# Optimization experiments

Hardware: AMD Instinct MI355X
Metric: run time of the kernel (lower is better)

## Reference

```python
import jax, jax.numpy as jnp
import numpy as np

N = 100000   # nodes
E = 1600000  # edges
IN_DIM, HID, HEADS, OUT_DIM = 8, 64, 4, 3


def _add_self_loops(src, dst, n):
    loop = jnp.arange(n, dtype=src.dtype)
    return jnp.concatenate([src, loop]), jnp.concatenate([dst, loop])


def gcn_conv(x, src, dst, n, W, b):
    # PyG GCNConv: add self-loops, symmetric normalization deg^-1/2 * deg^-1/2
    s, d = _add_self_loops(src, dst, n)
    deg = jax.ops.segment_sum(jnp.ones(s.shape[0], x.dtype), d, num_segments=n)
    dinv = jnp.where(deg > 0, jax.lax.rsqrt(deg), 0.0)
    norm = dinv[s] * dinv[d]                       # [E']
    h = x @ W                                      # [N, out]
    out = jax.ops.segment_sum(norm[:, None] * h[s], d, num_segments=n)
    return out + b


def gat_conv(x, src, dst, n, W, att_src, att_dst, b):
    # PyG GATConv, concat=True, negative_slope=0.2, self-loops added
    h = (x @ W).reshape(n, HEADS, HID)             # [N, H, C]
    s, d = _add_self_loops(src, dst, n)
    a_src = jnp.sum(h * att_src, axis=-1)          # [N, H]
    a_dst = jnp.sum(h * att_dst, axis=-1)          # [N, H]
    e = jax.nn.leaky_relu(a_src[s] + a_dst[d], negative_slope=0.2)  # [E', H]
    m = jax.lax.stop_gradient(jax.ops.segment_max(e, d, num_segments=n))
    ex = jnp.exp(e - m[d])
    denom = jax.ops.segment_sum(ex, d, num_segments=n)
    alpha = ex / (denom[d] + 1e-16)                # segment softmax over incoming edges
    out = jax.ops.segment_sum(alpha[:, :, None] * h[s], d, num_segments=n)  # [N, H, C]
    return out.reshape(n, HEADS * HID) + b


def setup_inputs() -> dict:
    key = jax.random.key(0)
    ks = jax.random.split(key, 16)
    def glorot(k, shape):
        fan = shape[0] + shape[-1]
        return jax.random.normal(k, shape, jnp.float32) * np.sqrt(2.0 / fan)
    return {
        "x": jax.random.normal(ks[0], (N, IN_DIM), jnp.float32),
        "edge_index": jax.random.randint(ks[1], (2, E), 0, N, jnp.int64 if jax.config.jax_enable_x64 else jnp.int32),
        "w1": glorot(ks[2], (IN_DIM, HID)), "b1": jnp.zeros((HID,), jnp.float32),
        "w2": glorot(ks[3], (HID, HID)),   "b2": jnp.zeros((HID,), jnp.float32),
        "w3": glorot(ks[4], (HID, HID)),   "b3": jnp.zeros((HID,), jnp.float32),
        "wg": glorot(ks[5], (HID, HEADS * HID)), "bg": jnp.zeros((HEADS * HID,), jnp.float32),
        "att_src": glorot(ks[6], (HEADS, HID)),
        "att_dst": glorot(ks[7], (HEADS, HID)),
        "wc1": glorot(ks[8], (HEADS * HID, HID)), "bc1": jnp.zeros((HID,), jnp.float32),
        "wc2": glorot(ks[9], (HID, OUT_DIM)),     "bc2": jnp.zeros((OUT_DIM,), jnp.float32),
    }


def reference(x, edge_index, w1, b1, w2, b2, w3, b3, wg, bg, att_src, att_dst, wc1, bc1, wc2, bc2):
    src, dst = edge_index[0], edge_index[1]
    n = x.shape[0]
    # stacked GCN convs with ReLU; residual when shapes match (layers 2,3)
    h = jax.nn.relu(gcn_conv(x, src, dst, n, w1, b1))
    h = h + jax.nn.relu(gcn_conv(h, src, dst, n, w2, b2))
    h = h + jax.nn.relu(gcn_conv(h, src, dst, n, w3, b3))
    # GAT attention layer (4 heads, concat)
    h_att = gat_conv(h, src, dst, n, wg, att_src, att_dst, bg)  # [N, 256]
    # classifier MLP (dropout is inference no-op)
    z = jax.nn.relu(h_att @ wc1 + bc1)
    logits = z @ wc2 + bc2
    return jax.nn.log_softmax(logits, axis=1)
```

## Files before the change

### kernel.cpp

```cpp
#include <hip/hip_runtime.h>
#include <math.h>


typedef _Float16 half8 __attribute__((ext_vector_type(8)));
typedef _Float16 f16x8 __attribute__((ext_vector_type(8)));
typedef float f32x4 __attribute__((ext_vector_type(4)));

__device__ __forceinline__ float leaky02(float v) { return v > 0.f ? v : 0.2f * v; }


template <int CTRL>
__device__ __forceinline__ float dpp_add(float v) {
    int iv = __builtin_bit_cast(int, v);
    int r = __builtin_amdgcn_update_dpp(iv, iv, CTRL, 0xF, 0xF, false);
    return v + __builtin_bit_cast(float, r);
}
template <int OFF>
__device__ __forceinline__ float swz_add(float v) {
    int r = __builtin_amdgcn_ds_swizzle(__builtin_bit_cast(int, v), OFF);
    return v + __builtin_bit_cast(float, r);
}
template <int CTRL>
__device__ __forceinline__ float dpp_max(float v) {
    int iv = __builtin_bit_cast(int, v);
    int r = __builtin_amdgcn_update_dpp(iv, iv, CTRL, 0xF, 0xF, false);
    return fmaxf(v, __builtin_bit_cast(float, r));
}
template <int OFF>
__device__ __forceinline__ float swz_max(float v) {
    int r = __builtin_amdgcn_ds_swizzle(__builtin_bit_cast(int, v), OFF);
    return fmaxf(v, __builtin_bit_cast(float, r));
}
__device__ __forceinline__ float red8(float v) {
    v = dpp_add<0xB1>(v);
    v = dpp_add<0x4E>(v);
    v = swz_add<0x101F>(v);
    return v;
}
__device__ __forceinline__ float red16(float v) {
    v = dpp_add<0xB1>(v);
    v = dpp_add<0x4E>(v);
    v = swz_add<0x101F>(v);
    v = dpp_add<0x128>(v);
    return v;
}
__device__ __forceinline__ float red64(float v) {
    v = dpp_add<0xB1>(v);
    v = dpp_add<0x4E>(v);
    v = swz_add<0x101F>(v);
    v = dpp_add<0x128>(v);
    v = swz_add<0x401F>(v);
    v = v + __shfl_xor(v, 32);
    return v;
}
__device__ __forceinline__ float red64max(float v) {
    v = dpp_max<0xB1>(v);
    v = dpp_max<0x4E>(v);
    v = swz_max<0x101F>(v);
    v = dpp_max<0x128>(v);
    v = swz_max<0x401F>(v);
    v = fmaxf(v, __shfl_xor(v, 32));
    return v;
}


__global__ void count_kernel(const int* __restrict__ dst, int E, int range,
                             int* __restrict__ counts) {
    int grp = blockIdx.x & 7;
    int nlo = grp * range;
    int nhi = nlo + range;
    int nblk = gridDim.x >> 3;
    int c = blockIdx.x >> 3;
    int stride = nblk * blockDim.x;
    for (int e = c * blockDim.x + threadIdx.x; e < E; e += stride) {
        int d = dst[e];
        if (d >= nlo && d < nhi) atomicAdd(&counts[d], 1);
    }
}

__global__ void scan_pass1(const int* __restrict__ counts, int n, int* __restrict__ blockSums) {
    __shared__ int sh[256];
    int base = blockIdx.x * 2048;
    int tid = threadIdx.x;
    int s = 0;
#pragma unroll
    for (int j = 0; j < 8; ++j) {
        int idx = base + tid * 8 + j;
        if (idx < n) s += counts[idx];
    }
    sh[tid] = s;
    __syncthreads();
    for (int off = 128; off > 0; off >>= 1) {
        if (tid < off) sh[tid] += sh[tid + off];
        __syncthreads();
    }
    if (tid == 0) blockSums[blockIdx.x] = sh[0];
}

__global__ void scan_pass2(const int* __restrict__ blockSums, int nb, int* __restrict__ blockOffs) {
    if (threadIdx.x == 0 && blockIdx.x == 0) {
        int run = 0;
        for (int i = 0; i < nb; ++i) { blockOffs[i] = run; run += blockSums[i]; }
    }
}

__global__ void scan_pass3(const int* __restrict__ counts, int n,
                           const int* __restrict__ blockOffs,
                           const float* __restrict__ x,
                           int* __restrict__ row_ptr, int* __restrict__ cursor,
                           float* __restrict__ dinv, float* __restrict__ rdinv,
                           _Float16* __restrict__ xs) {
    __shared__ int sh[256];
    int base = blockIdx.x * 2048;
    int tid = threadIdx.x;
    int cnt[8];
    int local = 0;
#pragma unroll
    for (int j = 0; j < 8; ++j) {
        int idx = base + tid * 8 + j;
        cnt[j] = (idx < n) ? counts[idx] : 0;
        local += cnt[j];
    }
    sh[tid] = local;
    __syncthreads();
    for (int off = 1; off < 256; off <<= 1) {
        int v = (tid >= off) ? sh[tid - off] : 0;
        __syncthreads();
        sh[tid] += v;
        __syncthreads();
    }
    int run = blockOffs[blockIdx.x] + sh[tid] - local;
#pragma unroll
    for (int j = 0; j < 8; ++j) {
        int idx = base + tid * 8 + j;
        if (idx < n) {
            row_ptr[idx] = run;
            cursor[idx] = run;
            float dv = rsqrtf((float)(cnt[j] + 1));
            dinv[idx] = dv;
            rdinv[idx] = sqrtf((float)(cnt[j] + 1));
#pragma unroll
            for (int t = 0; t < 8; ++t) xs[idx * 8 + t] = (_Float16)(dv * x[idx * 8 + t]);
            run += cnt[j];
            if (idx == n - 1) row_ptr[n] = run;
        }
    }
}

__global__ void scatter_kernel(const int* __restrict__ src, const int* __restrict__ dst,
                               int E, int range,
                               int* __restrict__ cursor, int* __restrict__ col_src) {
    int grp = blockIdx.x & 7;
    int nlo = grp * range;
    int nhi = nlo + range;
    int nblk = gridDim.x >> 3;
    int c = blockIdx.x >> 3;
    int stride = nblk * blockDim.x;
    for (int e = c * blockDim.x + threadIdx.x; e < E; e += stride) {
        int d = dst[e];
        if (d >= nlo && d < nhi) {
            int pos = atomicAdd(&cursor[d], 1);
            col_src[pos] = src[e];
        }
    }
}


__global__ void ccomb_kernel(const float* __restrict__ Wg, const float* __restrict__ bg,
                             const float* __restrict__ wc1, const float* __restrict__ bc1,
                             const float* __restrict__ att_src, const float* __restrict__ att_dst,
                             _Float16* __restrict__ CcombP, float* __restrict__ bcomb,
                             float* __restrict__ wse, float* __restrict__ wde) {
    int bid = blockIdx.x;
    int j = threadIdx.x;
    if (bid < 256) {
        int i = bid;
        float s = 0.f;
        for (int c = 0; c < 64; ++c)
            s += Wg[(i & 63) * 256 + (i >> 6) * 64 + c] * wc1[((i >> 6) * 64 + c) * 64 + j];
        _Float16 hi = (_Float16)s;
        _Float16 lo = (_Float16)(s - (float)hi);
        int kt = i >> 5, l = (((i >> 3) & 3) << 4) | (j & 15), e = i & 7, ct = j >> 4;
        CcombP[(ct * 8 + kt) * 512 + l * 8 + e] = hi;
        CcombP[(32 + ct * 8 + kt) * 512 + l * 8 + e] = lo;
    } else {
        float s = bc1[j];
        for (int i = 0; i < 256; ++i) s += bg[i] * wc1[i * 64 + j];
        bcomb[j] = s;
#pragma unroll
        for (int h = 0; h < 4; ++h) {
            float ss = 0.f, sd = 0.f;
            for (int c = 0; c < 64; ++c) {
                float w = Wg[j * 256 + h * 64 + c];
                ss += w * att_src[h * 64 + c];
                sd += w * att_dst[h * 64 + c];
            }
            wse[j * 4 + h] = ss;
            wde[j * 4 + h] = sd;
        }
    }
}


__global__ void gcn_layer1(const half8* __restrict__ xs8,
                           const float* __restrict__ W1, const float* __restrict__ b1,
                           const int* __restrict__ row_ptr, const int* __restrict__ col_src,
                           const float* __restrict__ dinv, int n,
                           _Float16* __restrict__ hs1) {
    int tid = threadIdx.x, lane = tid & 63, wid = tid >> 6;
    int node = blockIdx.x * 4 + wid;
    if (node >= n) return;
    int beg = row_ptr[node], end = row_ptr[node + 1];
    int deg = end - beg;
    float acc[8] = {0.f, 0.f, 0.f, 0.f, 0.f, 0.f, 0.f, 0.f};
    for (int base = 0; base < deg; base += 64) {
        int cs = col_src[min(beg + base + lane, end - 1)];
        half8 v = xs8[cs];
        if (base + lane < deg) {
#pragma unroll
            for (int c = 0; c < 8; ++c) acc[c] += (float)v[c];
        }
    }
#pragma unroll
    for (int c = 0; c < 8; ++c) acc[c] = red64(acc[c]);
    half8 sv = xs8[node];
    float di = dinv[node];
    float agg[8];
#pragma unroll
    for (int c = 0; c < 8; ++c) agg[c] = (acc[c] + (float)sv[c]) * di;
    float sum = b1[lane];
#pragma unroll
    for (int k = 0; k < 8; ++k) sum = fmaf(agg[k], W1[k * 64 + lane], sum);
    hs1[node * 64 + lane] = (_Float16)(di * fmaxf(sum, 0.f));
}


template <bool LAST>
__global__ void gcn_layer64(const _Float16* __restrict__ hs_in,
                            const float* __restrict__ W, const float* __restrict__ b,
                            const int* __restrict__ row_ptr, const int* __restrict__ col_src,
                            const float* __restrict__ dinv, const float* __restrict__ rdinv,
                            const float* __restrict__ wse, const float* __restrict__ wde,
                            int n,
                            _Float16* __restrict__ hout,
                            float4* __restrict__ a_src4, float4* __restrict__ a_dst4) {
    __shared__ float agg_lds[4][64];
    int tid = threadIdx.x;
    int lane = tid & 63;
    int wid = tid >> 6;
    int t = lane >> 3, g = lane & 7;
    const half8* hs8 = (const half8*)hs_in;
    float wreg[64];
#pragma unroll
    for (int k = 0; k < 64; ++k) wreg[k] = W[k * 64 + lane];
    float bl = b[lane];
    float4 we, wd;
    if (LAST) {
        we = ((const float4*)wse)[lane];
        wd = ((const float4*)wde)[lane];
    }
    int nw = gridDim.x * 4;
    for (int node = blockIdx.x * 4 + wid; node < n; node += nw) {
        int beg = row_ptr[node], end = row_ptr[node + 1];
        int deg = end - beg;
        half8 sv = hs8[node * 8 + t];
        float ac[8];
#pragma unroll
        for (int c = 0; c < 8; ++c) ac[c] = (g == 0) ? (float)sv[c] : 0.f;
        for (int base = 0; base < deg; base += 64) {
            int cs = col_src[min(beg + base + lane, end - 1)];
            int lim = min(deg - base, 64);
            auto bodyF = [&](int eo8) {
                int s = __shfl(cs, eo8 + g);
                half8 v = hs8[s * 8 + t];
#pragma unroll
                for (int c = 0; c < 8; ++c) ac[c] += (float)v[c];
            };
            auto bodyG = [&](int eo8) {
                int eo = eo8 + g;
                int s = __shfl(cs, eo);
                half8 v = hs8[s * 8 + t];
                if (eo < lim) {
#pragma unroll
                    for (int c = 0; c < 8; ++c) ac[c] += (float)v[c];
                }
            };
            int eo8 = 0;
            for (; eo8 + 16 <= lim; eo8 += 16) { bodyF(eo8); bodyF(eo8 + 8); }
            if (eo8 < lim) {
                bodyG(eo8);
                eo8 += 8;
                if (eo8 < lim) bodyG(eo8);
            }
        }
        float di = dinv[node];
#pragma unroll
        for (int c = 0; c < 8; ++c) ac[c] = red8(ac[c]) * di;
        if (g == 0) {
            *(float4*)&agg_lds[wid][t * 8]     = make_float4(ac[0], ac[1], ac[2], ac[3]);
            *(float4*)&agg_lds[wid][t * 8 + 4] = make_float4(ac[4], ac[5], ac[6], ac[7]);
        }
        __asm__ volatile("s_waitcnt lgkmcnt(0)" ::: "memory");
        float sum = bl;
#pragma unroll
        for (int k4 = 0; k4 < 16; ++k4) {
            float4 a4 = *(const float4*)&agg_lds[wid][k4 * 4];
            sum = fmaf(a4.x, wreg[k4 * 4 + 0], sum);
            sum = fmaf(a4.y, wreg[k4 * 4 + 1], sum);
            sum = fmaf(a4.z, wreg[k4 * 4 + 2], sum);
            sum = fmaf(a4.w, wreg[k4 * 4 + 3], sum);
        }
        float hprev = rdinv[node] * (float)sv[g];
        float hv = hprev + fmaxf(sum, 0.f);
        if (!LAST) {
            hout[node * 64 + lane] = (_Float16)(di * hv);
        } else {
            hout[node * 64 + lane] = (_Float16)hv;
            float vs0 = red64(hv * we.x), vs1 = red64(hv * we.y);
            float vs2 = red64(hv * we.z), vs3 = red64(hv * we.w);
            float vd0 = red64(hv * wd.x), vd1 = red64(hv * wd.y);
            float vd2 = red64(hv * wd.z), vd3 = red64(hv * wd.w);
            if (lane == 0) {
                a_src4[node] = make_float4(vs0, vs1, vs2, vs3);
                a_dst4[node] = make_float4(vd0, vd1, vd2, vd3);
            }
        }
    }
}


__global__ __launch_bounds__(256, 4) void gat_agg(
        const _Float16* __restrict__ h3,
        const float4* __restrict__ a_src4, const float4* __restrict__ a_dst4,
        const int* __restrict__ row_ptr, const int* __restrict__ col_src,
        int n, _Float16* __restrict__ aggout) {
    __shared__ _Float16 HsAll[4][32 * 72];
    __shared__ _Float16 wATAll[4][16 * 40];
    int tid = threadIdx.x, lane = tid & 63, wid = tid >> 6;
    int node = blockIdx.x * 4 + wid;
    if (node >= n) return;
    _Float16* Hs = HsAll[wid];
    _Float16* wAT = wATAll[wid];

    int q = lane >> 4, m16 = lane & 15;
    float4 ad = a_dst4[node];
    int beg = row_ptr[node], end = row_ptr[node + 1];
    int deg = end - beg;
    int nslots = deg + 1;

    int swz = q << 4;
    const _Float16* Bb0 = Hs + (size_t)q * 8 * 72 + ((0 * 16 + m16) ^ swz);
    const _Float16* Bb1 = Hs + (size_t)q * 8 * 72 + ((1 * 16 + m16) ^ swz);
    const _Float16* Bb2 = Hs + (size_t)q * 8 * 72 + ((2 * 16 + m16) ^ swz);
    const _Float16* Bb3 = Hs + (size_t)q * 8 * 72 + ((3 * 16 + m16) ^ swz);
    const f16x8* Ab = (const f16x8*)(wAT + m16 * 40 + q * 8);
    int c0 = (lane & 7) * 8;

    f32x4 acc0 = {0.f,0.f,0.f,0.f}, acc1 = {0.f,0.f,0.f,0.f};
    f32x4 acc2 = {0.f,0.f,0.f,0.f}, acc3 = {0.f,0.f,0.f,0.f};
    float dh0 = 0.f, dh1 = 0.f, dh2 = 0.f, dh3 = 0.f;
    float m0 = 0.f, m1 = 0.f, m2 = 0.f, m3 = 0.f;

    for (int base = 0; base < nslots; base += 32) {
        int sl = base + (lane & 31);
        int eidx = max(min(beg + sl - 1, end - 1), 0);
        int cs = (sl == 0) ? node : col_src[eidx];
        float4 as = a_src4[cs];
        float vm = (sl < nslots && lane < 32) ? 1.f : 0.f;
        float l0 = leaky02(as.x + ad.x);
        float l1 = leaky02(as.y + ad.y);
        float l2 = leaky02(as.z + ad.z);
        float l3 = leaky02(as.w + ad.w);
        if (base == 0) {
            m0 = red64max(vm > 0.f ? l0 : -1e30f);
            m1 = red64max(vm > 0.f ? l1 : -1e30f);
            m2 = red64max(vm > 0.f ? l2 : -1e30f);
            m3 = red64max(vm > 0.f ? l3 : -1e30f);
        }
        float w0 = vm * __expf(fminf(l0 - m0, 10.f));
        float w1 = vm * __expf(fminf(l1 - m1, 10.f));
        float w2 = vm * __expf(fminf(l2 - m2, 10.f));
        float w3 = vm * __expf(fminf(l3 - m3, 10.f));
        dh0 += w0; dh1 += w1; dh2 += w2; dh3 += w3;
        if (lane < 32) {
            int s32 = lane & 31;
            _Float16 h0 = (_Float16)w0, h1 = (_Float16)w1;
            _Float16 h2 = (_Float16)w2, h3v = (_Float16)w3;
            wAT[0 * 40 + s32] = h0;
            wAT[1 * 40 + s32] = h1;
            wAT[2 * 40 + s32] = h2;
            wAT[3 * 40 + s32] = h3v;
            wAT[4 * 40 + s32] = (_Float16)(w0 - (float)h0);
            wAT[5 * 40 + s32] = (_Float16)(w1 - (float)h1);
            wAT[6 * 40 + s32] = (_Float16)(w2 - (float)h2);
            wAT[7 * 40 + s32] = (_Float16)(w3 - (float)h3v);
        }
#pragma unroll
        for (int i = 0; i < 4; ++i) {
            int r = i * 8 + (lane >> 3);
            int s = __shfl(cs, r);
            half8 hv = *(const half8*)(h3 + (size_t)s * 64 + c0);
            *(half8*)(Hs + r * 72 + (c0 ^ (i << 4))) = hv;
        }
        __asm__ volatile("s_waitcnt lgkmcnt(0)" ::: "memory");
        f16x8 A = *Ab;
        f16x8 B0, B1, B2, B3;
#pragma unroll
        for (int e = 0; e < 8; ++e) {
            B0[e] = Bb0[e * 72];
            B1[e] = Bb1[e * 72];
            B2[e] = Bb2[e * 72];
            B3[e] = Bb3[e * 72];
        }
        acc0 = __builtin_amdgcn_mfma_f32_16x16x32_f16(A, B0, acc0, 0, 0, 0);
        acc1 = __builtin_amdgcn_mfma_f32_16x16x32_f16(A, B1, acc1, 0, 0, 0);
        acc2 = __builtin_amdgcn_mfma_f32_16x16x32_f16(A, B2, acc2, 0, 0, 0);
        acc3 = __builtin_amdgcn_mfma_f32_16x16x32_f16(A, B3, acc3, 0, 0, 0);
        __asm__ volatile("s_waitcnt lgkmcnt(0)" ::: "memory");
    }

    dh0 = red64(dh0); dh1 = red64(dh1); dh2 = red64(dh2); dh3 = red64(dh3);
    float rd[4];
    rd[0] = 1.f / (dh0 + 1e-16f);
    rd[1] = 1.f / (dh1 + 1e-16f);
    rd[2] = 1.f / (dh2 + 1e-16f);
    rd[3] = 1.f / (dh3 + 1e-16f);
    float tot[4][4];
#pragma unroll
    for (int r = 0; r < 4; ++r) {
        tot[0][r] = acc0[r] + __shfl_xor(acc0[r], 16);
        tot[1][r] = acc1[r] + __shfl_xor(acc1[r], 16);
        tot[2][r] = acc2[r] + __shfl_xor(acc2[r], 16);
        tot[3][r] = acc3[r] + __shfl_xor(acc3[r], 16);
    }
    if (lane < 16) {
        size_t ob = (size_t)node * 256 + lane;
#pragma unroll
        for (int r = 0; r < 4; ++r) {
#pragma unroll
            for (int ct = 0; ct < 4; ++ct)
                aggout[ob + r * 64 + ct * 16] = (_Float16)(tot[ct][r] * rd[r]);
        }
    }
}


__global__ __launch_bounds__(256) void mlp_mfma(
        const _Float16* __restrict__ agg,
        const _Float16* __restrict__ CP,
        const float* __restrict__ bcomb,
        const float* __restrict__ wc2, const float* __restrict__ bc2,
        int n, float* __restrict__ out) {
    __shared__ float part[4][16][3];
    int tid = threadIdx.x;
    int lane = tid & 63;
    int w = __builtin_amdgcn_readfirstlane(tid >> 6);
    int c16 = lane & 15, hi = lane >> 4;

    f16x8 bh[8], blo[8];
#pragma unroll
    for (int kt = 0; kt < 8; ++kt) {
        bh[kt]  = *(const f16x8*)(CP + (size_t)(w * 8 + kt) * 512 + lane * 8);
        blo[kt] = *(const f16x8*)(CP + (size_t)(32 + w * 8 + kt) * 512 + lane * 8);
    }
    int col = w * 16 + c16;
    float bc  = bcomb[col];
    float w20 = wc2[col * 3 + 0], w21 = wc2[col * 3 + 1], w22 = wc2[col * 3 + 2];
    float bb0 = bc2[0], bb1 = bc2[1], bb2 = bc2[2];

    int ntiles = (n + 15) >> 4;
    for (int tile = blockIdx.x; tile < ntiles; tile += gridDim.x) {
        int rowb = tile * 16;
        int row = min(rowb + c16, n - 1);
        const _Float16* ap = agg + (size_t)row * 256 + hi * 8;
        f16x8 a[8];
#pragma unroll
        for (int kt = 0; kt < 8; ++kt) a[kt] = *(const f16x8*)(ap + kt * 32);
        f32x4 acc = {0.f, 0.f, 0.f, 0.f};
#pragma unroll
        for (int kt = 0; kt < 8; ++kt) {
            acc = __builtin_amdgcn_mfma_f32_16x16x32_f16(a[kt], bh[kt],  acc, 0, 0, 0);
            acc = __builtin_amdgcn_mfma_f32_16x16x32_f16(a[kt], blo[kt], acc, 0, 0, 0);
        }
        float pr[4][3];
#pragma unroll
        for (int r = 0; r < 4; ++r) {
            float z = fmaxf(acc[r] + bc, 0.f);
            pr[r][0] = red16(z * w20);
            pr[r][1] = red16(z * w21);
            pr[r][2] = red16(z * w22);
        }
        if (c16 == 0) {
#pragma unroll
            for (int r = 0; r < 4; ++r) {
                part[w][hi * 4 + r][0] = pr[r][0];
                part[w][hi * 4 + r][1] = pr[r][1];
                part[w][hi * 4 + r][2] = pr[r][2];
            }
        }
        __syncthreads();
        if (tid < 16) {
            int node = rowb + tid;
            if (node < n) {
                float e0 = part[0][tid][0] + part[1][tid][0] + part[2][tid][0] + part[3][tid][0] + bb0;
                float e1 = part[0][tid][1] + part[1][tid][1] + part[2][tid][1] + part[3][tid][1] + bb1;
                float e2 = part[0][tid][2] + part[1][tid][2] + part[2][tid][2] + part[3][tid][2] + bb2;
                float mx = fmaxf(e0, fmaxf(e1, e2));
                float lse = mx + logf(expf(e0 - mx) + expf(e1 - mx) + expf(e2 - mx));
                out[(size_t)node * 3 + 0] = e0 - lse;
                out[(size_t)node * 3 + 1] = e1 - lse;
                out[(size_t)node * 3 + 2] = e2 - lse;
            }
        }
        __syncthreads();
    }
}


extern "C" void kernel_launch(void* const* d_in, const int* in_sizes, int n_in,
                              void* d_out, int out_size, void* d_ws, size_t ws_size,
                              hipStream_t stream) {
    const float* x       = (const float*)d_in[0];
    const int*   ei      = (const int*)d_in[1];
    const float* w1      = (const float*)d_in[2];
    const float* b1      = (const float*)d_in[3];
    const float* w2      = (const float*)d_in[4];
    const float* b2      = (const float*)d_in[5];
    const float* w3      = (const float*)d_in[6];
    const float* b3      = (const float*)d_in[7];
    const float* wg      = (const float*)d_in[8];
    const float* bg      = (const float*)d_in[9];
    const float* att_s   = (const float*)d_in[10];
    const float* att_d   = (const float*)d_in[11];
    const float* wc1     = (const float*)d_in[12];
    const float* bc1     = (const float*)d_in[13];
    const float* wc2     = (const float*)d_in[14];
    const float* bc2     = (const float*)d_in[15];
    float* out = (float*)d_out;

    const int N = in_sizes[0] / 8;
    const int E = in_sizes[1] / 2;
    const int* srcv = ei;
    const int* dstv = ei + E;

    char* ws = (char*)d_ws;
    size_t off = 0;
    auto alloc = [&](size_t bytes) -> char* {
        char* p = ws + off;
        off += (bytes + 255) & ~(size_t)255;
        return p;
    };
    int*      counts    = (int*)alloc((size_t)N * 4);
    int*      row_ptr   = (int*)alloc((size_t)(N + 1) * 4);
    int*      cursor    = (int*)alloc((size_t)N * 4);
    int*      col_src   = (int*)alloc((size_t)E * 4);
    int*      blockSums = (int*)alloc(4096 * 4);
    int*      blockOffs = (int*)alloc(4096 * 4);
    float*    dinv      = (float*)alloc((size_t)N * 4);
    float*    rdinv     = (float*)alloc((size_t)N * 4);
    _Float16* xs        = (_Float16*)alloc((size_t)N * 8 * 2);
    float*    a_src     = (float*)alloc((size_t)N * 16);
    float*    a_dst     = (float*)alloc((size_t)N * 16);
    float*    wse       = (float*)alloc(256 * 4);
    float*    wde       = (float*)alloc(256 * 4);
    _Float16* CcombP    = (_Float16*)alloc(64 * 1024);
    float*    bcomb     = (float*)alloc(64 * 4);
    _Float16* bufA      = (_Float16*)alloc((size_t)N * 64 * 2);
    _Float16* bufB      = (_Float16*)alloc((size_t)N * 64 * 2);
    _Float16* aggbuf    = (_Float16*)alloc((size_t)N * 256 * 2);
    _Float16* hs1 = bufA;
    _Float16* hs2 = bufB;
    _Float16* h3  = bufA;
    (void)ws_size; (void)n_in; (void)out_size;

    hipMemsetAsync(counts, 0, (size_t)N * 4, stream);

    const int TPB = 256;
    int range = (N + 7) / 8;
    count_kernel<<<1024, TPB, 0, stream>>>(dstv, E, range, counts);

    int NB = (N + 2047) / 2048;
    scan_pass1<<<NB, TPB, 0, stream>>>(counts, N, blockSums);
    scan_pass2<<<1, 64, 0, stream>>>(blockSums, NB, blockOffs);
    scan_pass3<<<NB, TPB, 0, stream>>>(counts, N, blockOffs, x,
                                       row_ptr, cursor, dinv, rdinv, xs);
    scatter_kernel<<<2048, TPB, 0, stream>>>(srcv, dstv, E, range, cursor, col_src);

    ccomb_kernel<<<257, 64, 0, stream>>>(wg, bg, wc1, bc1, att_s, att_d,
                                         CcombP, bcomb, wse, wde);

    int gridN = (N + 3) / 4;
    gcn_layer1<<<gridN, TPB, 0, stream>>>((const half8*)xs, w1, b1, row_ptr, col_src,
                                          dinv, N, hs1);
    const int G64 = 2048;
    gcn_layer64<false><<<G64, TPB, 0, stream>>>(hs1, w2, b2, row_ptr, col_src,
                                                dinv, rdinv, wse, wde, N, hs2,
                                                nullptr, nullptr);
    gcn_layer64<true><<<G64, TPB, 0, stream>>>(hs2, w3, b3, row_ptr, col_src,
                                               dinv, rdinv, wse, wde, N, h3,
                                               (float4*)a_src, (float4*)a_dst);

    gat_agg<<<gridN, TPB, 0, stream>>>(h3, (const float4*)a_src, (const float4*)a_dst,
                                       row_ptr, col_src, N, aggbuf);
    mlp_mfma<<<2048, TPB, 0, stream>>>(aggbuf, CcombP, bcomb, wc2, bc2, N, out);
}
```

Measured before the change: 551.5 us.

## Split GCN layers into gather kernel plus MFMA dense transform

```diff
diff --git a/kernel.cpp b/kernel.cpp
--- a/kernel.cpp
+++ b/kernel.cpp
@@ -169,8 +169,10 @@
 __global__ void ccomb_kernel(const float* __restrict__ Wg, const float* __restrict__ bg,
                              const float* __restrict__ wc1, const float* __restrict__ bc1,
                              const float* __restrict__ att_src, const float* __restrict__ att_dst,
+                             const float* __restrict__ w2, const float* __restrict__ w3,
                              _Float16* __restrict__ CcombP, float* __restrict__ bcomb,
-                             float* __restrict__ wse, float* __restrict__ wde) {
+                             float* __restrict__ wse, float* __restrict__ wde,
+                             _Float16* __restrict__ W2P, _Float16* __restrict__ W3P) {
     int bid = blockIdx.x;
     int j = threadIdx.x;
     if (bid < 256) {
@@ -183,7 +185,7 @@
         int kt = i >> 5, l = (((i >> 3) & 3) << 4) | (j & 15), e = i & 7, ct = j >> 4;
         CcombP[(ct * 8 + kt) * 512 + l * 8 + e] = hi;
         CcombP[(32 + ct * 8 + kt) * 512 + l * 8 + e] = lo;
-    } else {
+    } else if (bid == 256) {
         float s = bc1[j];
         for (int i = 0; i < 256; ++i) s += bg[i] * wc1[i * 64 + j];
         bcomb[j] = s;
@@ -198,6 +200,16 @@
             wse[j * 4 + h] = ss;
             wde[j * 4 + h] = sd;
         }
+    } else {
+        int i = (bid < 321) ? (bid - 257) : (bid - 321);
+        const float* W = (bid < 321) ? w2 : w3;
+        _Float16* WP = (bid < 321) ? W2P : W3P;
+        float s = W[i * 64 + j];
+        _Float16 hi = (_Float16)s;
+        _Float16 lo = (_Float16)(s - (float)hi);
+        int kt = i >> 5, l = (((i >> 3) & 3) << 4) | (j & 15), e = i & 7, ct = j >> 4;
+        WP[(ct * 2 + kt) * 512 + l * 8 + e] = hi;
+        WP[(8 + ct * 2 + kt) * 512 + l * 8 + e] = lo;
     }
 }
 
@@ -235,95 +247,144 @@
 }
 
 
+__global__ void gcn_agg(const _Float16* __restrict__ hs_in,
+                        const int* __restrict__ row_ptr, const int* __restrict__ col_src,
+                        const float* __restrict__ dinv, int n,
+                        _Float16* __restrict__ aggout) {
+    int tid = threadIdx.x, lane = tid & 63, wid = tid >> 6;
+    int node = blockIdx.x * 4 + wid;
+    if (node >= n) return;
+    int t = lane >> 3, g = lane & 7;
+    const half8* hs8 = (const half8*)hs_in;
+    int beg = row_ptr[node], end = row_ptr[node + 1];
+    int deg = end - beg;
+    half8 sv = hs8[node * 8 + t];
+    float ac[8];
+#pragma unroll
+    for (int c = 0; c < 8; ++c) ac[c] = (g == 0) ? (float)sv[c] : 0.f;
+    for (int base = 0; base < deg; base += 64) {
+        int cs = col_src[min(beg + base + lane, end - 1)];
+        int lim = min(deg - base, 64);
+        auto bodyF = [&](int eo8) {
+            int s = __shfl(cs, eo8 + g);
+            half8 v = hs8[s * 8 + t];
+#pragma unroll
+            for (int c = 0; c < 8; ++c) ac[c] += (float)v[c];
+        };
+        auto bodyG = [&](int eo8) {
+            int eo = eo8 + g;
+            int s = __shfl(cs, eo);
+            half8 v = hs8[s * 8 + t];
+            if (eo < lim) {
+#pragma unroll
+                for (int c = 0; c < 8; ++c) ac[c] += (float)v[c];
+            }
+        };
+        int eo8 = 0;
+        for (; eo8 + 16 <= lim; eo8 += 16) { bodyF(eo8); bodyF(eo8 + 8); }
+        if (eo8 < lim) {
+            bodyG(eo8);
+            eo8 += 8;
+            if (eo8 < lim) bodyG(eo8);
+        }
+    }
+    float di = dinv[node];
+#pragma unroll
+    for (int c = 0; c < 8; ++c) ac[c] = red8(ac[c]) * di;
+    if (g == 0) {
+        half8 hv;
+#pragma unroll
+        for (int c = 0; c < 8; ++c) hv[c] = (_Float16)ac[c];
+        *(half8*)(aggout + (size_t)node * 64 + t * 8) = hv;
+    }
+}
+
+
 template <bool LAST>
-__global__ void gcn_layer64(const _Float16* __restrict__ hs_in,
-                            const float* __restrict__ W, const float* __restrict__ b,
-                            const int* __restrict__ row_ptr, const int* __restrict__ col_src,
-                            const float* __restrict__ dinv, const float* __restrict__ rdinv,
-                            const float* __restrict__ wse, const float* __restrict__ wde,
-                            int n,
-                            _Float16* __restrict__ hout,
-                            float4* __restrict__ a_src4, float4* __restrict__ a_dst4) {
-    __shared__ float agg_lds[4][64];
+__global__ __launch_bounds__(256) void gcn_mfma(
+        const _Float16* __restrict__ agg,
+        const _Float16* __restrict__ WP,
+        const float* __restrict__ b,
+        const _Float16* __restrict__ hs_in,
+        const float* __restrict__ dinv, const float* __restrict__ rdinv,
+        const float* __restrict__ wse, const float* __restrict__ wde,
+        int n, _Float16* __restrict__ hout,
+        float4* __restrict__ a_src4, float4* __restrict__ a_dst4) {
+    __shared__ float partS[4][16][4];
+    __shared__ float partD[4][16][4];
     int tid = threadIdx.x;
     int lane = tid & 63;
-    int wid = tid >> 6;
-    int t = lane >> 3, g = lane & 7;
-    const half8* hs8 = (const half8*)hs_in;
-    float wreg[64];
-#pragma unroll
-    for (int k = 0; k < 64; ++k) wreg[k] = W[k * 64 + lane];
-    float bl = b[lane];
-    float4 we, wd;
+    int w = __builtin_amdgcn_readfirstlane(tid >> 6);
+    int c16 = lane & 15, hi = lane >> 4;
+
+    f16x8 bh[2], blo[2];
+#pragma unroll
+    for (int kt = 0; kt < 2; ++kt) {
+        bh[kt]  = *(const f16x8*)(WP + (size_t)(w * 2 + kt) * 512 + lane * 8);
+        blo[kt] = *(const f16x8*)(WP + (size_t)(8 + w * 2 + kt) * 512 + lane * 8);
+    }
+    int col = w * 16 + c16;
+    float bl = b[col];
+    float4 wev, wdv;
     if (LAST) {
-        we = ((const float4*)wse)[lane];
-        wd = ((const float4*)wde)[lane];
-    }
-    int nw = gridDim.x * 4;
-    for (int node = blockIdx.x * 4 + wid; node < n; node += nw) {
-        int beg = row_ptr[node], end = row_ptr[node + 1];
-        int deg = end - beg;
-        half8 sv = hs8[node * 8 + t];
-        float ac[8];
-#pragma unroll
-        for (int c = 0; c < 8; ++c) ac[c] = (g == 0) ? (float)sv[c] : 0.f;
-        for (int base = 0; base < deg; base += 64) {
-            int cs = col_src[min(beg + base + lane, end - 1)];
-            int lim = min(deg - base, 64);
-            auto bodyF = [&](int eo8) {
-                int s = __shfl(cs, eo8 + g);
-                half8 v = hs8[s * 8 + t];
-#pragma unroll
-                for (int c = 0; c < 8; ++c) ac[c] += (float)v[c];
-            };
-            auto bodyG = [&](int eo8) {
-                int eo = eo8 + g;
-                int s = __shfl(cs, eo);
-                half8 v = hs8[s * 8 + t];
-                if (eo < lim) {
-#pragma unroll
-                    for (int c = 0; c < 8; ++c) ac[c] += (float)v[c];
+        wev = ((const float4*)wse)[col];
+        wdv = ((const float4*)wde)[col];
+    }
+
+    int ntiles = (n + 15) >> 4;
+    for (int tile = blockIdx.x; tile < ntiles; tile += gridDim.x) {
+        int rowb = tile * 16;
+        int arow = min(rowb + c16, n - 1);
+        const _Float16* ap = agg + (size_t)arow * 64 + hi * 8;
+        f16x8 a0 = *(const f16x8*)(ap);
+        f16x8 a1 = *(const f16x8*)(ap + 32);
+        f32x4 acc = {0.f, 0.f, 0.f, 0.f};
+        acc = __builtin_amdgcn_mfma_f32_16x16x32_f16(a0, bh[0],  acc, 0, 0, 0);
+        acc = __builtin_amdgcn_mfma_f32_16x16x32_f16(a0, blo[0], acc, 0, 0, 0);
+        acc = __builtin_amdgcn_mfma_f32_16x16x32_f16(a1, bh[1],  acc, 0, 0, 0);
+        acc = __builtin_amdgcn_mfma_f32_16x16x32_f16(a1, blo[1], acc, 0, 0, 0);
+#pragma unroll
+        for (int r = 0; r < 4; ++r) {
+            int noder = rowb + hi * 4 + r;
+            bool ok = noder < n;
+            int ni = min(noder, n - 1);
+            float hp = rdinv[ni] * (float)hs_in[(size_t)ni * 64 + col];
+            float z = fmaxf(acc[r] + bl, 0.f);
+            float hv = hp + z;
+            if (!LAST) {
+                if (ok) hout[(size_t)ni * 64 + col] = (_Float16)(dinv[ni] * hv);
+            } else {
+                if (ok) hout[(size_t)ni * 64 + col] = (_Float16)hv;
+                float s0 = red16(hv * wev.x), s1 = red16(hv * wev.y);
+                float s2 = red16(hv * wev.z), s3 = red16(hv * wev.w);
+                float d0 = red16(hv * wdv.x), d1 = red16(hv * wdv.y);
+                float d2 = red16(hv * wdv.z), d3 = red16(hv * wdv.w);
+                if (c16 == 0) {
+                    *(float4*)&partS[w][hi * 4 + r][0] = make_float4(s0, s1, s2, s3);
+                    *(float4*)&partD[w][hi * 4 + r][0] = make_float4(d0, d1, d2, d3);
                 }
-            };
-            int eo8 = 0;
-            for (; eo8 + 16 <= lim; eo8 += 16) { bodyF(eo8); bodyF(eo8 + 8); }
-            if (eo8 < lim) {
-                bodyG(eo8);
-                eo8 += 8;
-                if (eo8 < lim) bodyG(eo8);
             }
         }
-        float di = dinv[node];
-#pragma unroll
-        for (int c = 0; c < 8; ++c) ac[c] = red8(ac[c]) * di;
-        if (g == 0) {
-            *(float4*)&agg_lds[wid][t * 8]     = make_float4(ac[0], ac[1], ac[2], ac[3]);
-            *(float4*)&agg_lds[wid][t * 8 + 4] = make_float4(ac[4], ac[5], ac[6], ac[7]);
-        }
-        __asm__ volatile("s_waitcnt lgkmcnt(0)" ::: "memory");
-        float sum = bl;
-#pragma unroll
-        for (int k4 = 0; k4 < 16; ++k4) {
-            float4 a4 = *(const float4*)&agg_lds[wid][k4 * 4];
-            sum = fmaf(a4.x, wreg[k4 * 4 + 0], sum);
-            sum = fmaf(a4.y, wreg[k4 * 4 + 1], sum);
-            sum = fmaf(a4.z, wreg[k4 * 4 + 2], sum);
-            sum = fmaf(a4.w, wreg[k4 * 4 + 3], sum);
-        }
-        float hprev = rdinv[node] * (float)sv[g];
-        float hv = hprev + fmaxf(sum, 0.f);
-        if (!LAST) {
-            hout[node * 64 + lane] = (_Float16)(di * hv);
-        } else {
-            hout[node * 64 + lane] = (_Float16)hv;
-            float vs0 = red64(hv * we.x), vs1 = red64(hv * we.y);
-            float vs2 = red64(hv * we.z), vs3 = red64(hv * we.w);
-            float vd0 = red64(hv * wd.x), vd1 = red64(hv * wd.y);
-            float vd2 = red64(hv * wd.z), vd3 = red64(hv * wd.w);
-            if (lane == 0) {
-                a_src4[node] = make_float4(vs0, vs1, vs2, vs3);
-                a_dst4[node] = make_float4(vd0, vd1, vd2, vd3);
+        if (LAST) {
+            __syncthreads();
+            if (tid < 16) {
+                int node = rowb + tid;
+                if (node < n) {
+                    float4 s = make_float4(
+                        partS[0][tid][0] + partS[1][tid][0] + partS[2][tid][0] + partS[3][tid][0],
+                        partS[0][tid][1] + partS[1][tid][1] + partS[2][tid][1] + partS[3][tid][1],
+                        partS[0][tid][2] + partS[1][tid][2] + partS[2][tid][2] + partS[3][tid][2],
+                        partS[0][tid][3] + partS[1][tid][3] + partS[2][tid][3] + partS[3][tid][3]);
+                    float4 d = make_float4(
+                        partD[0][tid][0] + partD[1][tid][0] + partD[2][tid][0] + partD[3][tid][0],
+                        partD[0][tid][1] + partD[1][tid][1] + partD[2][tid][1] + partD[3][tid][1],
+                        partD[0][tid][2] + partD[1][tid][2] + partD[2][tid][2] + partD[3][tid][2],
+                        partD[0][tid][3] + partD[1][tid][3] + partD[2][tid][3] + partD[3][tid][3]);
+                    a_src4[node] = s;
+                    a_dst4[node] = d;
+                }
             }
+            __syncthreads();
         }
     }
 }
@@ -565,12 +626,15 @@
     float*    wde       = (float*)alloc(256 * 4);
     _Float16* CcombP    = (_Float16*)alloc(64 * 1024);
     float*    bcomb     = (float*)alloc(64 * 4);
+    _Float16* W2P       = (_Float16*)alloc(16 * 1024);
+    _Float16* W3P       = (_Float16*)alloc(16 * 1024);
     _Float16* bufA      = (_Float16*)alloc((size_t)N * 64 * 2);
     _Float16* bufB      = (_Float16*)alloc((size_t)N * 64 * 2);
     _Float16* aggbuf    = (_Float16*)alloc((size_t)N * 256 * 2);
     _Float16* hs1 = bufA;
     _Float16* hs2 = bufB;
     _Float16* h3  = bufA;
+    _Float16* aggA = aggbuf;
     (void)ws_size; (void)n_in; (void)out_size;
 
     hipMemsetAsync(counts, 0, (size_t)N * 4, stream);
@@ -586,19 +650,21 @@
                                        row_ptr, cursor, dinv, rdinv, xs);
     scatter_kernel<<<2048, TPB, 0, stream>>>(srcv, dstv, E, range, cursor, col_src);
 
-    ccomb_kernel<<<257, 64, 0, stream>>>(wg, bg, wc1, bc1, att_s, att_d,
-                                         CcombP, bcomb, wse, wde);
+    ccomb_kernel<<<385, 64, 0, stream>>>(wg, bg, wc1, bc1, att_s, att_d, w2, w3,
+                                         CcombP, bcomb, wse, wde, W2P, W3P);
 
     int gridN = (N + 3) / 4;
     gcn_layer1<<<gridN, TPB, 0, stream>>>((const half8*)xs, w1, b1, row_ptr, col_src,
                                           dinv, N, hs1);
-    const int G64 = 2048;
-    gcn_layer64<false><<<G64, TPB, 0, stream>>>(hs1, w2, b2, row_ptr, col_src,
-                                                dinv, rdinv, wse, wde, N, hs2,
-                                                nullptr, nullptr);
-    gcn_layer64<true><<<G64, TPB, 0, stream>>>(hs2, w3, b3, row_ptr, col_src,
-                                               dinv, rdinv, wse, wde, N, h3,
-                                               (float4*)a_src, (float4*)a_dst);
+
+    gcn_agg<<<gridN, TPB, 0, stream>>>(hs1, row_ptr, col_src, dinv, N, aggA);
+    gcn_mfma<false><<<2048, TPB, 0, stream>>>(aggA, W2P, b2, hs1, dinv, rdinv,
+                                              nullptr, nullptr, N, hs2,
+                                              nullptr, nullptr);
+    gcn_agg<<<gridN, TPB, 0, stream>>>(hs2, row_ptr, col_src, dinv, N, aggA);
+    gcn_mfma<true><<<2048, TPB, 0, stream>>>(aggA, W3P, b3, hs2, dinv, rdinv,
+                                             wse, wde, N, h3,
+                                             (float4*)a_src, (float4*)a_dst);
 
     gat_agg<<<gridN, TPB, 0, stream>>>(h3, (const float4*)a_src, (const float4*)a_dst,
                                        row_ptr, col_src, N, aggbuf);
```

After: 522.5 us. -5.3%, faster.
